# Kernel optimization log

Hardware: AMD Instinct MI355X
Metric: run time of the kernel (lower is better)

## Reference

```python
import jax, jax.numpy as jnp
import numpy as np

N_FFT = 1024
HOP = 256
BATCH = 16
SAMPLES = 262144


def hann_window(n):
    # torch.hann_window default (periodic=True): 0.5 * (1 - cos(2*pi*k/n))
    k = jnp.arange(n, dtype=jnp.float32)
    return 0.5 - 0.5 * jnp.cos(2.0 * jnp.pi * k / n)


def setup_inputs() -> dict:
    key = jax.random.key(0)
    x = jax.random.normal(key, (BATCH, SAMPLES), dtype=jnp.float32)
    window = hann_window(N_FFT)  # (n_fft,)
    return {"x": x, "window": window}


def reference(x, window):
    # Faithful STFT.forward: pad -> frame (identity-kernel conv1d == gather) ->
    # window -> rfft along the frame axis; norm=None.
    pad = N_FFT - HOP
    pad_left = pad // 2
    xp = jnp.pad(x, ((0, 0), (pad_left, pad - pad_left)))
    n_frames = (xp.shape[1] - N_FFT) // HOP + 1
    # gather-based framing, equivalent to conv1d with eye(n_fft) kernel, stride=hop
    idx = jnp.arange(n_frames)[:, None] * HOP + jnp.arange(N_FFT)[None, :]  # (frames, n_fft)
    frames = xp[:, idx]                       # (B, frames, n_fft)
    frames = frames * window[None, None, :]   # windowing
    spec = jnp.fft.rfft(frames, axis=-1)      # (B, frames, n_bins)
    real = jnp.transpose(spec.real, (0, 2, 1))  # (B, n_bins, frames)
    imag = jnp.transpose(spec.imag, (0, 2, 1))
    return real, imag
```

## Files before the change

### kernel.cpp

```cpp
#include <hip/hip_runtime.h>

#define HOP      256
#define SAMPLES  262144
#define NBINS    513
#define NFRAMES  1024
#define FPB      16

__device__ __forceinline__ float2 cmul(float2 a, float2 b) {
  return make_float2(a.x * b.x - a.y * b.y, a.x * b.y + a.y * b.x);
}

__device__ __forceinline__ void fft8(float2 v[8]) {
  const float R = 0.70710678118654752440f;
  float2 s0 = make_float2(v[0].x + v[4].x, v[0].y + v[4].y);
  float2 d0 = make_float2(v[0].x - v[4].x, v[0].y - v[4].y);
  float2 s1 = make_float2(v[1].x + v[5].x, v[1].y + v[5].y);
  float2 d1 = make_float2(v[1].x - v[5].x, v[1].y - v[5].y);
  float2 s2 = make_float2(v[2].x + v[6].x, v[2].y + v[6].y);
  float2 d2 = make_float2(v[2].x - v[6].x, v[2].y - v[6].y);
  float2 s3 = make_float2(v[3].x + v[7].x, v[3].y + v[7].y);
  float2 d3 = make_float2(v[3].x - v[7].x, v[3].y - v[7].y);
  float2 e1 = make_float2(R * (d1.x + d1.y), R * (d1.y - d1.x));
  float2 e2 = make_float2(d2.y, -d2.x);
  float2 e3 = make_float2(R * (d3.y - d3.x), R * (-d3.x - d3.y));
  float2 p0 = make_float2(s0.x + s2.x, s0.y + s2.y);
  float2 q0 = make_float2(s0.x - s2.x, s0.y - s2.y);
  float2 p1 = make_float2(s1.x + s3.x, s1.y + s3.y);
  float2 q1 = make_float2(s1.x - s3.x, s1.y - s3.y);
  float2 q1t = make_float2(q1.y, -q1.x);
  float2 p2 = make_float2(d0.x + e2.x, d0.y + e2.y);
  float2 q2 = make_float2(d0.x - e2.x, d0.y - e2.y);
  float2 p3 = make_float2(e1.x + e3.x, e1.y + e3.y);
  float2 q3 = make_float2(e1.x - e3.x, e1.y - e3.y);
  float2 q3t = make_float2(q3.y, -q3.x);
  v[0] = make_float2(p0.x + p1.x, p0.y + p1.y);
  v[4] = make_float2(p0.x - p1.x, p0.y - p1.y);
  v[2] = make_float2(q0.x + q1t.x, q0.y + q1t.y);
  v[6] = make_float2(q0.x - q1t.x, q0.y - q1t.y);
  v[1] = make_float2(p2.x + p3.x, p2.y + p3.y);
  v[5] = make_float2(p2.x - p3.x, p2.y - p3.y);
  v[3] = make_float2(q2.x + q3t.x, q2.y + q3t.y);
  v[7] = make_float2(q2.x - q3t.x, q2.y - q3t.y);
}

__device__ __forceinline__ int swz(int c) {
  int H = c >> 6, M = (c >> 3) & 7, L = c & 7;
  return (H << 6) | ((M ^ (H & 1)) << 3) | (L ^ M);
}

__global__ __launch_bounds__(1024)
void stft_kernel(const float* __restrict__ x, const float* __restrict__ win,
                 float* __restrict__ out) {
  __shared__ float2 z[FPB * 512];
  const int t  = threadIdx.x;
  const int b  = blockIdx.x >> 6;
  const int f0 = (blockIdx.x & 63) * FPB;

  {
    const int w = t >> 6;
    const int u = t & 63;
    const int fr = f0 + w;
    const float* xb = x + (size_t)b * SAMPLES;
    const int base = fr * HOP - 384;
    float2* zf = z + w * 512;

    float2 r[8];
#pragma unroll
    for (int n1 = 0; n1 < 8; ++n1) {
      int s = 2 * (64 * n1 + u);
      int idx = base + s;
      float2 xv = make_float2(0.f, 0.f);
      if (idx >= 0 && idx < SAMPLES) xv = *(const float2*)(xb + idx);
      float2 wv = *(const float2*)(win + s);
      r[n1] = make_float2(xv.x * wv.x, xv.y * wv.y);
    }

    fft8(r);
    float sn, cs;
    __sincosf((float)u * (-6.28318530717958647693f / 512.f), &sn, &cs);
    float2 wb = make_float2(cs, sn), tw = wb;
#pragma unroll
    for (int k1 = 1; k1 < 8; ++k1) {
      r[k1] = cmul(r[k1], tw);
      if (k1 < 7) tw = cmul(tw, wb);
    }
#pragma unroll
    for (int k1 = 0; k1 < 8; ++k1) zf[swz((k1 << 6) | u) ^ w] = r[k1];

    const int g = u >> 3, m2 = u & 7;
    float2 y[8];
#pragma unroll
    for (int m1 = 0; m1 < 8; ++m1) y[m1] = zf[swz((g << 6) | (m1 << 3) | m2) ^ w];

    fft8(y);
    __sincosf((float)m2 * (-6.28318530717958647693f / 64.f), &sn, &cs);
    wb = make_float2(cs, sn); tw = wb;
#pragma unroll
    for (int j1 = 1; j1 < 8; ++j1) {
      y[j1] = cmul(y[j1], tw);
      if (j1 < 7) tw = cmul(tw, wb);
    }
#pragma unroll
    for (int j1 = 0; j1 < 8; ++j1) zf[swz((g << 6) | (j1 << 3) | m2) ^ w] = y[j1];

    const int j1 = u & 7;
    float2 h[8];
#pragma unroll
    for (int m = 0; m < 8; ++m) h[m] = zf[swz((g << 6) | (j1 << 3) | m) ^ w];

    fft8(h);
#pragma unroll
    for (int j2 = 0; j2 < 8; ++j2) zf[swz(g | (j1 << 3) | (j2 << 6)) ^ w] = h[j2];
  }
  __syncthreads();

  {
    const int f  = t & 15;
    const int q  = t >> 4;
    const int fr = f0 + f;
    const float2* zf = z + f * 512;
    float* out_r = out;
    float* out_i = out + (size_t)16 * NBINS * NFRAMES;
    float sn, cs;
    __sincosf((float)q * (-6.28318530717958647693f / 1024.f), &sn, &cs);
    float2 tw = make_float2(cs, sn);
    const float2 stp = make_float2(0.92387953251128675613f, -0.38268343236508977173f);
#pragma unroll
    for (int i = 0; i < 9; ++i) {
      int k = q + (i << 6);
      if (k > 512) break;
      float2 Zk = zf[swz(k & 511) ^ f];
      float2 Zm = zf[swz((512 - k) & 511) ^ f];
      float xer  = 0.5f * (Zk.x + Zm.x);
      float xei  = 0.5f * (Zk.y - Zm.y);
      float xor_ = 0.5f * (Zk.y + Zm.y);
      float xoi  = -0.5f * (Zk.x - Zm.x);
      float xr = xer + tw.x * xor_ - tw.y * xoi;
      float xi = xei + tw.x * xoi + tw.y * xor_;
      size_t o = ((size_t)b * NBINS + k) * NFRAMES + fr;
      out_r[o] = xr;
      out_i[o] = xi;
      tw = cmul(tw, stp);
    }
  }
}

extern "C" void kernel_launch(void* const* d_in, const int* in_sizes, int n_in,
                              void* d_out, int out_size, void* d_ws, size_t ws_size,
                              hipStream_t stream) {
  const float* x = (const float*)d_in[0];
  const float* w = (const float*)d_in[1];
  float* out = (float*)d_out;
  (void)in_sizes; (void)n_in; (void)out_size; (void)d_ws; (void)ws_size;
  stft_kernel<<<dim3(1024), dim3(1024), 0, stream>>>(x, w, out);
}
```

Before: 28.30 us.

## Emit conjugate-symmetric bin pairs together, use power twiddles, and raise occupancy hint

The real-FFT post-processing loop now handles bins k and 512-k in one iteration, deriving the second bin from the same Zk/Zm pair and twiddle. This halves the shared-memory reads and twiddle recurrence steps per output. The stage twiddles are built as powers of the base twiddle instead of one serial multiply chain, which shortens the dependency chain. A second `__launch_bounds__` argument asks for 8 waves per EU, which caps registers and may cause spills.

```diff
diff --git a/kernel.cpp b/kernel.cpp
--- a/kernel.cpp
+++ b/kernel.cpp
@@ -48,7 +48,7 @@
   return (H << 6) | ((M ^ (H & 1)) << 3) | (L ^ M);
 }
 
-__global__ __launch_bounds__(1024)
+__global__ __launch_bounds__(1024, 8)
 void stft_kernel(const float* __restrict__ x, const float* __restrict__ win,
                  float* __restrict__ out) {
   __shared__ float2 z[FPB * 512];
@@ -78,11 +78,18 @@
     fft8(r);
     float sn, cs;
     __sincosf((float)u * (-6.28318530717958647693f / 512.f), &sn, &cs);
-    float2 wb = make_float2(cs, sn), tw = wb;
-#pragma unroll
-    for (int k1 = 1; k1 < 8; ++k1) {
-      r[k1] = cmul(r[k1], tw);
-      if (k1 < 7) tw = cmul(tw, wb);
+    {
+      float2 w1 = make_float2(cs, sn);
+      float2 w2 = cmul(w1, w1);
+      float2 w3 = cmul(w2, w1);
+      float2 w4 = cmul(w2, w2);
+      r[1] = cmul(r[1], w1);
+      r[2] = cmul(r[2], w2);
+      r[3] = cmul(r[3], w3);
+      r[4] = cmul(r[4], w4);
+      r[5] = cmul(r[5], cmul(w4, w1));
+      r[6] = cmul(r[6], cmul(w4, w2));
+      r[7] = cmul(r[7], cmul(w4, w3));
     }
 #pragma unroll
     for (int k1 = 0; k1 < 8; ++k1) zf[swz((k1 << 6) | u) ^ w] = r[k1];
@@ -94,11 +101,18 @@
 
     fft8(y);
     __sincosf((float)m2 * (-6.28318530717958647693f / 64.f), &sn, &cs);
-    wb = make_float2(cs, sn); tw = wb;
-#pragma unroll
-    for (int j1 = 1; j1 < 8; ++j1) {
-      y[j1] = cmul(y[j1], tw);
-      if (j1 < 7) tw = cmul(tw, wb);
+    {
+      float2 w1 = make_float2(cs, sn);
+      float2 w2 = cmul(w1, w1);
+      float2 w3 = cmul(w2, w1);
+      float2 w4 = cmul(w2, w2);
+      y[1] = cmul(y[1], w1);
+      y[2] = cmul(y[2], w2);
+      y[3] = cmul(y[3], w3);
+      y[4] = cmul(y[4], w4);
+      y[5] = cmul(y[5], cmul(w4, w1));
+      y[6] = cmul(y[6], cmul(w4, w2));
+      y[7] = cmul(y[7], cmul(w4, w3));
     }
 #pragma unroll
     for (int j1 = 0; j1 < 8; ++j1) zf[swz((g << 6) | (j1 << 3) | m2) ^ w] = y[j1];
@@ -126,20 +140,23 @@
     float2 tw = make_float2(cs, sn);
     const float2 stp = make_float2(0.92387953251128675613f, -0.38268343236508977173f);
 #pragma unroll
-    for (int i = 0; i < 9; ++i) {
+    for (int i = 0; i < 5; ++i) {
       int k = q + (i << 6);
-      if (k > 512) break;
-      float2 Zk = zf[swz(k & 511) ^ f];
+      if (k > 256) break;
+      float2 Zk = zf[swz(k) ^ f];
       float2 Zm = zf[swz((512 - k) & 511) ^ f];
       float xer  = 0.5f * (Zk.x + Zm.x);
       float xei  = 0.5f * (Zk.y - Zm.y);
       float xor_ = 0.5f * (Zk.y + Zm.y);
       float xoi  = -0.5f * (Zk.x - Zm.x);
-      float xr = xer + tw.x * xor_ - tw.y * xoi;
-      float xi = xei + tw.x * xoi + tw.y * xor_;
-      size_t o = ((size_t)b * NBINS + k) * NFRAMES + fr;
-      out_r[o] = xr;
-      out_i[o] = xi;
+      float ur = tw.x * xor_ - tw.y * xoi;
+      float ui = tw.x * xoi + tw.y * xor_;
+      size_t o1 = ((size_t)b * NBINS + k) * NFRAMES + fr;
+      size_t o2 = ((size_t)b * NBINS + (512 - k)) * NFRAMES + fr;
+      out_r[o1] = xer + ur;
+      out_i[o1] = xei + ui;
+      out_r[o2] = xer - ur;
+      out_i[o2] = ui - xei;
       tw = cmul(tw, stp);
     }
   }
```

Result: faster. 27.72 us (-2.1%).
